# Performance work log

Hardware: AMD Instinct MI355X
Metric: run time of the kernel (lower is better)

## Reference

```python
import jax, jax.numpy as jnp
import numpy as np

WS = (7, 7)          # window size
N = WS[0] * WS[1]    # 49 tokens per window
C = 128              # dim
H = 4                # num heads
D = C // H           # head dim = 32
B = 8192             # batch * num_windows
NW = 1024            # windows per image
SCALE = D ** -0.5


def _relative_position_index():
    coords_h = np.arange(WS[0])
    coords_w = np.arange(WS[1])
    coords = np.stack(np.meshgrid(coords_h, coords_w, indexing='ij'))  # [2,Wh,Ww]
    flat = coords.reshape(2, -1)                                        # [2,N]
    rel = flat[:, :, None] - flat[:, None, :]                           # [2,N,N]
    rel = rel.transpose(1, 2, 0).astype(np.int64)                       # [N,N,2]
    rel[:, :, 0] += WS[0] - 1
    rel[:, :, 1] += WS[1] - 1
    rel[:, :, 0] *= 2 * WS[1] - 1
    return rel.sum(-1)                                                  # [N,N]


def setup_inputs() -> dict:
    key = jax.random.key(0)
    ks = jax.random.split(key, 8)
    s = 0.02
    return {
        'x': jax.random.normal(ks[0], (B, N, C), jnp.float32),
        'y': jax.random.normal(ks[1], (B, N, C), jnp.float32),
        'mask': jnp.zeros((NW, N, N), jnp.float32),
        'Wq': jax.random.normal(ks[2], (C, C), jnp.float32) * s,
        'bq': jnp.zeros((C,), jnp.float32),
        'Wkv': jax.random.normal(ks[3], (C, 2 * C), jnp.float32) * s,
        'bkv': jnp.zeros((2 * C,), jnp.float32),
        'bias_table': jax.random.normal(ks[4], ((2 * WS[0] - 1) * (2 * WS[1] - 1), H), jnp.float32) * s,
        'Wp': jax.random.normal(ks[5], (C, C), jnp.float32) * s,
        'bp': jnp.zeros((C,), jnp.float32),
        'rel_idx': jnp.asarray(_relative_position_index(), jnp.int32),
    }


def reference(x, y, mask, Wq, bq, Wkv, bkv, bias_table, Wp, bp, rel_idx):
    b = x.shape[0]
    # q/kv projections
    q = (x @ Wq + bq).reshape(b, N, H, D).transpose(0, 2, 1, 3) * SCALE   # [B,H,N,D]
    kv = (y @ Wkv + bkv).reshape(b, N, 2, H, D).transpose(2, 0, 3, 1, 4)  # [2,B,H,N,D]
    k, v = kv[0], kv[1]
    attn = jnp.einsum('bhnd,bhmd->bhnm', q, k)                            # [B,H,N,N]
    # relative position bias gather
    bias = bias_table[rel_idx.reshape(-1)].reshape(N, N, H).transpose(2, 0, 1)  # [H,N,N]
    attn = attn + bias[None]
    # mask add per window
    nW = mask.shape[0]
    attn = attn.reshape(b // nW, nW, H, N, N) + mask[None, :, None]
    attn = attn.reshape(b, H, N, N)
    attn = jax.nn.softmax(attn, axis=-1)
    out = jnp.einsum('bhnm,bhmd->bhnd', attn, v)                          # [B,H,N,D]
    out = out.transpose(0, 2, 1, 3).reshape(b, N, C)
    return out @ Wp + bp
```

## Files before the change

### kernel.cpp

```cpp
#include <hip/hip_runtime.h>
#include <cstddef>


#define MFMA16 __builtin_amdgcn_mfma_f32_16x16x32_bf16

typedef float f32x4 __attribute__((ext_vector_type(4)));
typedef __bf16 bf16x8 __attribute__((ext_vector_type(8)));
typedef unsigned short u16x8 __attribute__((ext_vector_type(8)));

constexpr int NTOK = 49;
constexpr int CDIM = 128;
constexpr int NWIN = 1024;
constexpr int NB = 8192;
constexpr float SCALE_F = 0.17677669529663687f;

__device__ __forceinline__ unsigned short f2bf(float f) {
  unsigned int u = __builtin_bit_cast(unsigned int, f);
  u += 0x7FFFu + ((u >> 16) & 1u);
  return (unsigned short)(u >> 16);
}

__device__ __forceinline__ int sw128(int row, int col) {
  return (row << 8) + ((((col >> 3) ^ row) & 15) << 4) + ((col & 7) << 1);
}
__device__ __forceinline__ int sw64(int row, int col) {
  return (row << 7) + ((((col >> 3) ^ (row >> 1)) & 7) << 4) + ((col & 7) << 1);
}

__global__ void prepack_kernel(const float* __restrict__ Wq, const float* __restrict__ Wkv,
                               const float* __restrict__ Wp, const float* __restrict__ bias_table,
                               const int* __restrict__ rel_idx,
                               unsigned short* __restrict__ wWq, unsigned short* __restrict__ wWk,
                               unsigned short* __restrict__ wWv, unsigned short* __restrict__ wWp,
                               float* __restrict__ wBias) {
  int t = blockIdx.x * 256 + threadIdx.x;
  int n = t >> 7, k = t & 127;
  wWq[t] = f2bf(Wq[k * 128 + n]);
  wWk[t] = f2bf(Wkv[k * 256 + n]);
  wWv[t] = f2bf(Wkv[k * 256 + 128 + n]);
  wWp[t] = f2bf(Wp[k * 128 + n]);
  if (t < 2401) {
    int r = rel_idx[t];
#pragma unroll
    for (int h = 0; h < 4; ++h) wBias[h * 2401 + t] = bias_table[r * 4 + h];
  }
}

__device__ __forceinline__ void stage_w(unsigned char* lds, const unsigned short* __restrict__ wsrc,
                                        int half, int tid) {
  const uint4* src = (const uint4*)(wsrc + half * 8192);
  uint4* dst = (uint4*)(lds + 49152);
#pragma unroll
  for (int it = 0; it < 4; ++it) {
    int i = tid + it * 256;
    int lr = i >> 4;
    dst[(lr << 4) | ((i ^ lr) & 15)] = src[i];
  }
}

template <int TGT>
__device__ __forceinline__ void p1_compute(unsigned char* lds, const bf16x8 af[4],
                                           const float* __restrict__ biasv, int half, int w,
                                           int li, int q4) {
#pragma unroll
  for (int ntl = 0; ntl < 4; ++ntl) {
    f32x4 acc = {0.f, 0.f, 0.f, 0.f};
#pragma unroll
    for (int ks = 0; ks < 4; ++ks) {
      bf16x8 bfr = *(const bf16x8*)(lds + 49152 + sw128(ntl * 16 + li, ks * 32 + q4 * 8));
      acc = MFMA16(af[ks], bfr, acc, 0, 0, 0);
    }
    const int n = half * 64 + ntl * 16 + li;
    const float bv = biasv[n];
#pragma unroll
    for (int r = 0; r < 4; ++r) {
      const int m = w * 16 + q4 * 4 + r;
      const unsigned short us = f2bf(acc[r] + bv);
      if (TGT == 0)
        *(unsigned short*)(lds + sw128(m, n)) = us;
      else if (TGT == 1)
        *(unsigned short*)(lds + 16384 + sw128(m, n)) = us;
      else
        *(unsigned short*)(lds + 32768 + sw64(n, m)) = us;
    }
  }
}

__global__ __launch_bounds__(256, 2) void attn_kernel(
    const float* __restrict__ x, const float* __restrict__ y, const float* __restrict__ mask,
    const float* __restrict__ bq, const float* __restrict__ bkv, const float* __restrict__ bp,
    const unsigned short* __restrict__ wWq, const unsigned short* __restrict__ wWk,
    const unsigned short* __restrict__ wWv, const unsigned short* __restrict__ wWp,
    const float* __restrict__ wBias, float* __restrict__ out) {
  __shared__ __align__(16) unsigned char lds[65536];
  const int tid = threadIdx.x;
  const int w = tid >> 6;
  const int lane = tid & 63;
  const int li = lane & 15;
  const int q4 = lane >> 4;
  const int b = blockIdx.x;

  bf16x8 ax[4], ay[4];
  {
    const int mrow = w * 16 + li;
    const bool mv = mrow < NTOK;
    const float* xr = x + ((size_t)b * NTOK + (mv ? mrow : 0)) * CDIM;
    const float* yr = y + ((size_t)b * NTOK + (mv ? mrow : 0)) * CDIM;
#pragma unroll
    for (int ks = 0; ks < 4; ++ks) {
      const int c0 = ks * 32 + q4 * 8;
      float4 a0 = *(const float4*)(xr + c0);
      float4 a1 = *(const float4*)(xr + c0 + 4);
      float4 b0 = *(const float4*)(yr + c0);
      float4 b1 = *(const float4*)(yr + c0 + 4);
      if (!mv) {
        a0.x = a0.y = a0.z = a0.w = 0.f; a1.x = a1.y = a1.z = a1.w = 0.f;
        b0.x = b0.y = b0.z = b0.w = 0.f; b1.x = b1.y = b1.z = b1.w = 0.f;
      }
      u16x8 ta, tb;
      ta[0] = f2bf(a0.x); ta[1] = f2bf(a0.y); ta[2] = f2bf(a0.z); ta[3] = f2bf(a0.w);
      ta[4] = f2bf(a1.x); ta[5] = f2bf(a1.y); ta[6] = f2bf(a1.z); ta[7] = f2bf(a1.w);
      tb[0] = f2bf(b0.x); tb[1] = f2bf(b0.y); tb[2] = f2bf(b0.z); tb[3] = f2bf(b0.w);
      tb[4] = f2bf(b1.x); tb[5] = f2bf(b1.y); tb[6] = f2bf(b1.z); tb[7] = f2bf(b1.w);
      ax[ks] = __builtin_bit_cast(bf16x8, ta);
      ay[ks] = __builtin_bit_cast(bf16x8, tb);
    }
  }

  stage_w(lds, wWq, 0, tid); __syncthreads();
  p1_compute<0>(lds, ax, bq, 0, w, li, q4); __syncthreads();
  stage_w(lds, wWq, 1, tid); __syncthreads();
  p1_compute<0>(lds, ax, bq, 1, w, li, q4); __syncthreads();
  stage_w(lds, wWk, 0, tid); __syncthreads();
  p1_compute<1>(lds, ay, bkv, 0, w, li, q4); __syncthreads();
  stage_w(lds, wWk, 1, tid); __syncthreads();
  p1_compute<1>(lds, ay, bkv, 1, w, li, q4); __syncthreads();
  stage_w(lds, wWv, 0, tid); __syncthreads();
  p1_compute<2>(lds, ay, bkv + 128, 0, w, li, q4); __syncthreads();
  stage_w(lds, wWv, 1, tid); __syncthreads();
  p1_compute<2>(lds, ay, bkv + 128, 1, w, li, q4); __syncthreads();

  const int h = w;
  const int PS = h * 8192;
  f32x4 s[4][4];
  {
    bf16x8 aq[4], bk[4];
#pragma unroll
    for (int mt = 0; mt < 4; ++mt)
      aq[mt] = *(const bf16x8*)(lds + sw128(mt * 16 + li, h * 32 + q4 * 8));
#pragma unroll
    for (int nt = 0; nt < 4; ++nt)
      bk[nt] = *(const bf16x8*)(lds + 16384 + sw128(nt * 16 + li, h * 32 + q4 * 8));
    const f32x4 zz = {0.f, 0.f, 0.f, 0.f};
#pragma unroll
    for (int mt = 0; mt < 4; ++mt)
#pragma unroll
      for (int nt = 0; nt < 4; ++nt) s[mt][nt] = MFMA16(aq[mt], bk[nt], zz, 0, 0, 0);
  }
  const float* __restrict__ maskw = mask + (size_t)(b & (NWIN - 1)) * 2401;
  const float* __restrict__ biash = wBias + h * 2401;
#pragma unroll
  for (int mt = 0; mt < 4; ++mt) {
#pragma unroll
    for (int r = 0; r < 4; ++r) {
      const int m = mt * 16 + q4 * 4 + r;
      const bool mvld = m < NTOK;
      const int mo = (mvld ? m : 0) * NTOK;
      float vv[4];
#pragma unroll
      for (int nt = 0; nt < 4; ++nt) {
        const int n = nt * 16 + li;
        float t = SCALE_F * s[mt][nt][r];
        if (n < NTOK) {
          if (mvld) t += biash[mo + n] + maskw[mo + n];
        } else {
          t = -1e30f;
        }
        vv[nt] = t;
      }
      float mx = fmaxf(fmaxf(vv[0], vv[1]), fmaxf(vv[2], vv[3]));
      mx = fmaxf(mx, __shfl_xor(mx, 1, 16));
      mx = fmaxf(mx, __shfl_xor(mx, 2, 16));
      mx = fmaxf(mx, __shfl_xor(mx, 4, 16));
      mx = fmaxf(mx, __shfl_xor(mx, 8, 16));
      float sm = 0.f;
#pragma unroll
      for (int nt = 0; nt < 4; ++nt) {
        vv[nt] = __expf(vv[nt] - mx);
        sm += vv[nt];
      }
      sm += __shfl_xor(sm, 1, 16);
      sm += __shfl_xor(sm, 2, 16);
      sm += __shfl_xor(sm, 4, 16);
      sm += __shfl_xor(sm, 8, 16);
      const float inv = __builtin_amdgcn_rcpf(sm);
#pragma unroll
      for (int nt = 0; nt < 4; ++nt) s[mt][nt][r] = vv[nt] * inv;
    }
  }
  __syncthreads();
#pragma unroll
  for (int mt = 0; mt < 4; ++mt)
#pragma unroll
    for (int r = 0; r < 4; ++r) {
      const int m = mt * 16 + q4 * 4 + r;
#pragma unroll
      for (int nt = 0; nt < 4; ++nt)
        *(unsigned short*)(lds + PS + sw64(m, nt * 16 + li)) = f2bf(s[mt][nt][r]);
    }

  f32x4 o[4][2];
  {
    bf16x8 ap[4][2], bv2[2][2];
#pragma unroll
    for (int mt = 0; mt < 4; ++mt)
#pragma unroll
      for (int ks = 0; ks < 2; ++ks)
        ap[mt][ks] = *(const bf16x8*)(lds + PS + sw64(mt * 16 + li, ks * 32 + q4 * 8));
#pragma unroll
    for (int nti = 0; nti < 2; ++nti)
#pragma unroll
      for (int ks = 0; ks < 2; ++ks)
        bv2[nti][ks] =
            *(const bf16x8*)(lds + 32768 + sw64(h * 32 + nti * 16 + li, ks * 32 + q4 * 8));
#pragma unroll
    for (int mt = 0; mt < 4; ++mt)
#pragma unroll
      for (int nti = 0; nti < 2; ++nti) {
        f32x4 acc = {0.f, 0.f, 0.f, 0.f};
#pragma unroll
        for (int ks = 0; ks < 2; ++ks) acc = MFMA16(ap[mt][ks], bv2[nti][ks], acc, 0, 0, 0);
        o[mt][nti] = acc;
      }
  }
  __syncthreads();

#pragma unroll
  for (int mt = 0; mt < 4; ++mt)
#pragma unroll
    for (int nti = 0; nti < 2; ++nti)
#pragma unroll
      for (int r = 0; r < 4; ++r) {
        const int m = mt * 16 + q4 * 4 + r;
        const int c = h * 32 + nti * 16 + li;
        *(unsigned short*)(lds + sw128(m, c)) = f2bf(o[mt][nti][r]);
      }
  stage_w(lds, wWp, 0, tid);
  __syncthreads();

  bf16x8 az[4];
#pragma unroll
  for (int ks = 0; ks < 4; ++ks)
    az[ks] = *(const bf16x8*)(lds + sw128(w * 16 + li, ks * 32 + q4 * 8));
#pragma unroll
  for (int half = 0; half < 2; ++half) {
    if (half == 1) {
      __syncthreads();
      stage_w(lds, wWp, 1, tid);
      __syncthreads();
    }
#pragma unroll
    for (int ntl = 0; ntl < 4; ++ntl) {
      f32x4 acc = {0.f, 0.f, 0.f, 0.f};
#pragma unroll
      for (int ks = 0; ks < 4; ++ks) {
        bf16x8 bw = *(const bf16x8*)(lds + 49152 + sw128(ntl * 16 + li, ks * 32 + q4 * 8));
        acc = MFMA16(az[ks], bw, acc, 0, 0, 0);
      }
      const int n = half * 64 + ntl * 16 + li;
      const float bpv = bp[n];
#pragma unroll
      for (int r = 0; r < 4; ++r) {
        const int m = w * 16 + q4 * 4 + r;
        if (m < NTOK) out[((size_t)b * NTOK + m) * CDIM + n] = acc[r] + bpv;
      }
    }
  }
}

extern "C" void kernel_launch(void* const* d_in, const int* in_sizes, int n_in, void* d_out,
                              int out_size, void* d_ws, size_t ws_size, hipStream_t stream) {
  const float* x = (const float*)d_in[0];
  const float* y = (const float*)d_in[1];
  const float* mask = (const float*)d_in[2];
  const float* Wq = (const float*)d_in[3];
  const float* bq = (const float*)d_in[4];
  const float* Wkv = (const float*)d_in[5];
  const float* bkv = (const float*)d_in[6];
  const float* bt = (const float*)d_in[7];
  const float* Wp = (const float*)d_in[8];
  const float* bp = (const float*)d_in[9];
  const int* rel = (const int*)d_in[10];
  float* out = (float*)d_out;

  unsigned short* wWq = (unsigned short*)d_ws;
  unsigned short* wWk = wWq + 16384;
  unsigned short* wWv = wWq + 32768;
  unsigned short* wWp = wWq + 49152;
  float* wBias = (float*)((char*)d_ws + 131072);

  prepack_kernel<<<64, 256, 0, stream>>>(Wq, Wkv, Wp, bt, rel, wWq, wWk, wWv, wWp, wBias);
  attn_kernel<<<NB, 256, 0, stream>>>(x, y, mask, bq, bkv, bp, wWq, wWk, wWv, wWp, wBias, out);
}
```

Measured before the change: 788.0 us.

## Load pre-packed MFMA weight fragments from global memory instead of staging through LDS

Weights are now prepacked into per-lane MFMA B-fragment order so each wave loads its fragments straight from global memory (L2-resident) rather than staging halves into LDS between barriers. Warps are remapped to a 2x2 (row-half, column-half) tiling so each weight fragment is reused across two row tiles. This removes the many stage/sync pairs and the 16KB weight staging area, shrinking LDS to 48KB and raising launch bounds to 3 blocks per CU. The cost is more global/L2 fragment traffic per block and higher register use for the doubled activation fragments.

```diff
diff --git a/kernel.cpp b/kernel.cpp
--- a/kernel.cpp
+++ b/kernel.cpp
@@ -30,79 +30,56 @@
 __global__ void prepack_kernel(const float* __restrict__ Wq, const float* __restrict__ Wkv,
                                const float* __restrict__ Wp, const float* __restrict__ bias_table,
                                const int* __restrict__ rel_idx,
-                               unsigned short* __restrict__ wWq, unsigned short* __restrict__ wWk,
-                               unsigned short* __restrict__ wWv, unsigned short* __restrict__ wWp,
-                               float* __restrict__ wBias) {
+                               unsigned short* __restrict__ wFrag, float* __restrict__ wBias) {
   int t = blockIdx.x * 256 + threadIdx.x;
-  int n = t >> 7, k = t & 127;
-  wWq[t] = f2bf(Wq[k * 128 + n]);
-  wWk[t] = f2bf(Wkv[k * 256 + n]);
-  wWv[t] = f2bf(Wkv[k * 256 + 128 + n]);
-  wWp[t] = f2bf(Wp[k * 128 + n]);
-  if (t < 2401) {
-    int r = rel_idx[t];
-#pragma unroll
-    for (int h = 0; h < 4; ++h) wBias[h * 2401 + t] = bias_table[r * 4 + h];
-  }
-}
-
-__device__ __forceinline__ void stage_w(unsigned char* lds, const unsigned short* __restrict__ wsrc,
-                                        int half, int tid) {
-  const uint4* src = (const uint4*)(wsrc + half * 8192);
-  uint4* dst = (uint4*)(lds + 49152);
-#pragma unroll
-  for (int it = 0; it < 4; ++it) {
-    int i = tid + it * 256;
-    int lr = i >> 4;
-    dst[(lr << 4) | ((i ^ lr) & 15)] = src[i];
-  }
-}
-
-template <int TGT>
-__device__ __forceinline__ void p1_compute(unsigned char* lds, const bf16x8 af[4],
-                                           const float* __restrict__ biasv, int half, int w,
-                                           int li, int q4) {
-#pragma unroll
-  for (int ntl = 0; ntl < 4; ++ntl) {
-    f32x4 acc = {0.f, 0.f, 0.f, 0.f};
-#pragma unroll
-    for (int ks = 0; ks < 4; ++ks) {
-      bf16x8 bfr = *(const bf16x8*)(lds + 49152 + sw128(ntl * 16 + li, ks * 32 + q4 * 8));
-      acc = MFMA16(af[ks], bfr, acc, 0, 0, 0);
-    }
-    const int n = half * 64 + ntl * 16 + li;
-    const float bv = biasv[n];
-#pragma unroll
-    for (int r = 0; r < 4; ++r) {
-      const int m = w * 16 + q4 * 4 + r;
-      const unsigned short us = f2bf(acc[r] + bv);
-      if (TGT == 0)
-        *(unsigned short*)(lds + sw128(m, n)) = us;
-      else if (TGT == 1)
-        *(unsigned short*)(lds + 16384 + sw128(m, n)) = us;
-      else
-        *(unsigned short*)(lds + 32768 + sw64(n, m)) = us;
-    }
-  }
-}
-
-__global__ __launch_bounds__(256, 2) void attn_kernel(
+  if (t < 8192) {
+    const int mat = t >> 11;
+    const int g = t & 2047;
+    const int frag = g >> 6, lane = g & 63;
+    const int nt = frag >> 2, ks = frag & 3;
+    const int li = lane & 15, q4 = lane >> 4;
+    const int n = nt * 16 + li;
+    u16x8 tmp;
+#pragma unroll
+    for (int j = 0; j < 8; ++j) {
+      const int k = ks * 32 + q4 * 8 + j;
+      float v;
+      if (mat == 0) v = Wq[k * 128 + n];
+      else if (mat == 1) v = Wkv[k * 256 + n];
+      else if (mat == 2) v = Wkv[k * 256 + 128 + n];
+      else v = Wp[k * 128 + n];
+      tmp[j] = f2bf(v);
+    }
+    *(u16x8*)(wFrag + (size_t)t * 8) = tmp;
+  } else {
+    const int tb = t - 8192;
+    if (tb < 2401) {
+      const int r = rel_idx[tb];
+#pragma unroll
+      for (int h = 0; h < 4; ++h) wBias[h * 2401 + tb] = bias_table[r * 4 + h];
+    }
+  }
+}
+
+__global__ __launch_bounds__(256, 3) void attn_kernel(
     const float* __restrict__ x, const float* __restrict__ y, const float* __restrict__ mask,
     const float* __restrict__ bq, const float* __restrict__ bkv, const float* __restrict__ bp,
-    const unsigned short* __restrict__ wWq, const unsigned short* __restrict__ wWk,
-    const unsigned short* __restrict__ wWv, const unsigned short* __restrict__ wWp,
-    const float* __restrict__ wBias, float* __restrict__ out) {
-  __shared__ __align__(16) unsigned char lds[65536];
+    const unsigned short* __restrict__ wFrag, const float* __restrict__ wBias,
+    float* __restrict__ out) {
+  __shared__ __align__(16) unsigned char lds[49152];
   const int tid = threadIdx.x;
   const int w = tid >> 6;
   const int lane = tid & 63;
   const int li = lane & 15;
   const int q4 = lane >> 4;
   const int b = blockIdx.x;
-
-  bf16x8 ax[4], ay[4];
-  {
-    const int mrow = w * 16 + li;
+  const int mh = w >> 1;
+  const int nh = w & 1;
+
+  bf16x8 ax[2][4], ay[2][4];
+#pragma unroll
+  for (int t = 0; t < 2; ++t) {
+    const int mrow = mh * 32 + t * 16 + li;
     const bool mv = mrow < NTOK;
     const float* xr = x + ((size_t)b * NTOK + (mv ? mrow : 0)) * CDIM;
     const float* yr = y + ((size_t)b * NTOK + (mv ? mrow : 0)) * CDIM;
@@ -122,23 +99,77 @@
       ta[4] = f2bf(a1.x); ta[5] = f2bf(a1.y); ta[6] = f2bf(a1.z); ta[7] = f2bf(a1.w);
       tb[0] = f2bf(b0.x); tb[1] = f2bf(b0.y); tb[2] = f2bf(b0.z); tb[3] = f2bf(b0.w);
       tb[4] = f2bf(b1.x); tb[5] = f2bf(b1.y); tb[6] = f2bf(b1.z); tb[7] = f2bf(b1.w);
-      ax[ks] = __builtin_bit_cast(bf16x8, ta);
-      ay[ks] = __builtin_bit_cast(bf16x8, tb);
-    }
-  }
-
-  stage_w(lds, wWq, 0, tid); __syncthreads();
-  p1_compute<0>(lds, ax, bq, 0, w, li, q4); __syncthreads();
-  stage_w(lds, wWq, 1, tid); __syncthreads();
-  p1_compute<0>(lds, ax, bq, 1, w, li, q4); __syncthreads();
-  stage_w(lds, wWk, 0, tid); __syncthreads();
-  p1_compute<1>(lds, ay, bkv, 0, w, li, q4); __syncthreads();
-  stage_w(lds, wWk, 1, tid); __syncthreads();
-  p1_compute<1>(lds, ay, bkv, 1, w, li, q4); __syncthreads();
-  stage_w(lds, wWv, 0, tid); __syncthreads();
-  p1_compute<2>(lds, ay, bkv + 128, 0, w, li, q4); __syncthreads();
-  stage_w(lds, wWv, 1, tid); __syncthreads();
-  p1_compute<2>(lds, ay, bkv + 128, 1, w, li, q4); __syncthreads();
+      ax[t][ks] = __builtin_bit_cast(bf16x8, ta);
+      ay[t][ks] = __builtin_bit_cast(bf16x8, tb);
+    }
+  }
+
+  const unsigned short* wq = wFrag + 0 * 16384 + nh * 8192;
+  const unsigned short* wk = wFrag + 1 * 16384 + nh * 8192;
+  const unsigned short* wv = wFrag + 2 * 16384 + nh * 8192;
+  const unsigned short* wp = wFrag + 3 * 16384 + nh * 8192;
+
+#pragma unroll
+  for (int ntl = 0; ntl < 4; ++ntl) {
+    bf16x8 wf[4];
+#pragma unroll
+    for (int ks = 0; ks < 4; ++ks)
+      wf[ks] = *(const bf16x8*)(wq + (ntl * 4 + ks) * 512 + lane * 8);
+    const int n = nh * 64 + ntl * 16 + li;
+    const float bv = bq[n];
+#pragma unroll
+    for (int t = 0; t < 2; ++t) {
+      f32x4 acc = {0.f, 0.f, 0.f, 0.f};
+#pragma unroll
+      for (int ks = 0; ks < 4; ++ks) acc = MFMA16(ax[t][ks], wf[ks], acc, 0, 0, 0);
+#pragma unroll
+      for (int r = 0; r < 4; ++r) {
+        const int m = mh * 32 + t * 16 + q4 * 4 + r;
+        *(unsigned short*)(lds + sw128(m, n)) = f2bf(acc[r] + bv);
+      }
+    }
+  }
+#pragma unroll
+  for (int ntl = 0; ntl < 4; ++ntl) {
+    bf16x8 wf[4];
+#pragma unroll
+    for (int ks = 0; ks < 4; ++ks)
+      wf[ks] = *(const bf16x8*)(wk + (ntl * 4 + ks) * 512 + lane * 8);
+    const int n = nh * 64 + ntl * 16 + li;
+    const float bv = bkv[n];
+#pragma unroll
+    for (int t = 0; t < 2; ++t) {
+      f32x4 acc = {0.f, 0.f, 0.f, 0.f};
+#pragma unroll
+      for (int ks = 0; ks < 4; ++ks) acc = MFMA16(ay[t][ks], wf[ks], acc, 0, 0, 0);
+#pragma unroll
+      for (int r = 0; r < 4; ++r) {
+        const int m = mh * 32 + t * 16 + q4 * 4 + r;
+        *(unsigned short*)(lds + 16384 + sw128(m, n)) = f2bf(acc[r] + bv);
+      }
+    }
+  }
+#pragma unroll
+  for (int ntl = 0; ntl < 4; ++ntl) {
+    bf16x8 wf[4];
+#pragma unroll
+    for (int ks = 0; ks < 4; ++ks)
+      wf[ks] = *(const bf16x8*)(wv + (ntl * 4 + ks) * 512 + lane * 8);
+    const int n = nh * 64 + ntl * 16 + li;
+    const float bv = bkv[128 + n];
+#pragma unroll
+    for (int t = 0; t < 2; ++t) {
+      f32x4 acc = {0.f, 0.f, 0.f, 0.f};
+#pragma unroll
+      for (int ks = 0; ks < 4; ++ks) acc = MFMA16(ay[t][ks], wf[ks], acc, 0, 0, 0);
+#pragma unroll
+      for (int r = 0; r < 4; ++r) {
+        const int m = mh * 32 + t * 16 + q4 * 4 + r;
+        *(unsigned short*)(lds + 32768 + sw64(n, m)) = f2bf(acc[r] + bv);
+      }
+    }
+  }
+  __syncthreads();
 
   const int h = w;
   const int PS = h * 8192;
@@ -245,33 +276,30 @@
         const int c = h * 32 + nti * 16 + li;
         *(unsigned short*)(lds + sw128(m, c)) = f2bf(o[mt][nti][r]);
       }
-  stage_w(lds, wWp, 0, tid);
   __syncthreads();
 
-  bf16x8 az[4];
-#pragma unroll
-  for (int ks = 0; ks < 4; ++ks)
-    az[ks] = *(const bf16x8*)(lds + sw128(w * 16 + li, ks * 32 + q4 * 8));
-#pragma unroll
-  for (int half = 0; half < 2; ++half) {
-    if (half == 1) {
-      __syncthreads();
-      stage_w(lds, wWp, 1, tid);
-      __syncthreads();
-    }
-#pragma unroll
-    for (int ntl = 0; ntl < 4; ++ntl) {
+  bf16x8 az[2][4];
+#pragma unroll
+  for (int t = 0; t < 2; ++t)
+#pragma unroll
+    for (int ks = 0; ks < 4; ++ks)
+      az[t][ks] = *(const bf16x8*)(lds + sw128(mh * 32 + t * 16 + li, ks * 32 + q4 * 8));
+#pragma unroll
+  for (int ntl = 0; ntl < 4; ++ntl) {
+    bf16x8 wf[4];
+#pragma unroll
+    for (int ks = 0; ks < 4; ++ks)
+      wf[ks] = *(const bf16x8*)(wp + (ntl * 4 + ks) * 512 + lane * 8);
+    const int n = nh * 64 + ntl * 16 + li;
+    const float bpv = bp[n];
+#pragma unroll
+    for (int t = 0; t < 2; ++t) {
       f32x4 acc = {0.f, 0.f, 0.f, 0.f};
 #pragma unroll
-      for (int ks = 0; ks < 4; ++ks) {
-        bf16x8 bw = *(const bf16x8*)(lds + 49152 + sw128(ntl * 16 + li, ks * 32 + q4 * 8));
-        acc = MFMA16(az[ks], bw, acc, 0, 0, 0);
-      }
-      const int n = half * 64 + ntl * 16 + li;
-      const float bpv = bp[n];
-#pragma unroll
-      for (int r = 0; r < 4; ++r) {
-        const int m = w * 16 + q4 * 4 + r;
+      for (int ks = 0; ks < 4; ++ks) acc = MFMA16(az[t][ks], wf[ks], acc, 0, 0, 0);
+#pragma unroll
+      for (int r = 0; r < 4; ++r) {
+        const int m = mh * 32 + t * 16 + q4 * 4 + r;
         if (m < NTOK) out[((size_t)b * NTOK + m) * CDIM + n] = acc[r] + bpv;
       }
     }
@@ -293,12 +321,9 @@
   const int* rel = (const int*)d_in[10];
   float* out = (float*)d_out;
 
-  unsigned short* wWq = (unsigned short*)d_ws;
-  unsigned short* wWk = wWq + 16384;
-  unsigned short* wWv = wWq + 32768;
-  unsigned short* wWp = wWq + 49152;
+  unsigned short* wFrag = (unsigned short*)d_ws;
   float* wBias = (float*)((char*)d_ws + 131072);
 
-  prepack_kernel<<<64, 256, 0, stream>>>(Wq, Wkv, Wp, bt, rel, wWq, wWk, wWv, wWp, wBias);
-  attn_kernel<<<NB, 256, 0, stream>>>(x, y, mask, bq, bkv, bp, wWq, wWk, wWv, wWp, wBias, out);
-}
+  prepack_kernel<<<64, 256, 0, stream>>>(Wq, Wkv, Wp, bt, rel, wFrag, wBias);
+  attn_kernel<<<NB, 256, 0, stream>>>(x, y, mask, bq, bkv, bp, wFrag, wBias, out);
+}
```

After: 752.2 us. 4.5% less time.
